# Performance work log

Measured on AMD Instinct MI355X. Metric: run time of the kernel, lower is better.

## Reference

```python
import jax, jax.numpy as jnp
import numpy as np

N_MELS = 80
FORMANT_START, FORMANT_END = 10, 50
W_L1, W_DELTA, W_DELTA2, W_SC, W_BAND, FORMANT_W = 1.0, 0.5, 0.25, 0.5, 1.0, 2.0
EPS = 1e-8


def _masked_mean(x, mask):
    # mask broadcasts to x's shape; count = sum of the broadcast mask
    n = jnp.maximum(jnp.sum(jnp.broadcast_to(mask, x.shape)), 1.0)
    return jnp.sum(x * mask) / n


def setup_inputs() -> dict:
    key = jax.random.key(0)
    k1, k2, k3 = jax.random.split(key, 3)
    B, T, D = 64, 4000, N_MELS
    pred_mel = jax.random.normal(k1, (B, T, D), dtype=jnp.float32)
    target_mel = jax.random.normal(k2, (B, T, D), dtype=jnp.float32)
    lengths = jax.random.randint(k3, (B,), T // 2, T + 1)
    mel_mask = (jnp.arange(T)[None, :] < lengths[:, None]).astype(jnp.float32)
    band_weights = jnp.ones((D,), dtype=jnp.float32).at[FORMANT_START:FORMANT_END].set(FORMANT_W)
    return {"pred_mel": pred_mel, "target_mel": target_mel, "mel_mask": mel_mask,
            "band_weights": band_weights}


def reference(pred_mel, target_mel, mel_mask, band_weights):
    mask3 = mel_mask[:, :, None]                      # (B,T,1)

    l1 = jnp.abs(pred_mel - target_mel)               # (B,T,D)
    l1_loss = _masked_mean(l1, mask3)

    # 1st-order deltas
    dp = pred_mel[:, 1:] - pred_mel[:, :-1]
    dt = target_mel[:, 1:] - target_mel[:, :-1]
    dmask = (mel_mask[:, 1:] * mel_mask[:, :-1])[:, :, None]
    delta_loss = _masked_mean(jnp.abs(dp - dt), dmask)

    # 2nd-order deltas
    d2p = dp[:, 1:] - dp[:, :-1]
    d2t = dt[:, 1:] - dt[:, :-1]
    d2mask = (mel_mask[:, 2:] * mel_mask[:, 1:-1] * mel_mask[:, :-2])[:, :, None]
    delta2_loss = _masked_mean(jnp.abs(d2p - d2t), d2mask)

    # spectral convergence
    diff = (pred_mel - target_mel) * mask3
    tgt_m = target_mel * mask3
    n = jnp.maximum(jnp.sum(jnp.broadcast_to(mask3, pred_mel.shape)), 1.0)
    sc_num = jnp.sqrt(jnp.sum(diff * diff) / n)
    sc_den = jnp.maximum(jnp.sqrt(jnp.sum(tgt_m * tgt_m) / n), EPS)
    sc_loss = sc_num / sc_den

    # band-weighted L1
    w = band_weights[None, None, :]
    band_loss = _masked_mean(l1 * w, mask3) / jnp.mean(band_weights)

    # energy (per-frame mean over mel bins)
    e_l1 = jnp.abs(pred_mel.mean(axis=-1) - target_mel.mean(axis=-1))  # (B,T)
    energy_loss = _masked_mean(e_l1, mel_mask)

    return (W_L1 * l1_loss + W_DELTA * delta_loss + W_DELTA2 * delta2_loss
            + W_SC * sc_loss + W_BAND * band_loss + 0.5 * energy_loss)
```

## Files before the change

kernel.cpp:

```cpp
#include <hip/hip_runtime.h>
#include <math.h>

#define D_MELS  80
#define T_DIM   4000
#define F4_ROW  20
#define NQ      10
#define NTHR    256
#define WPB     (NTHR / 64)
#define RPW     16
#define LDSROWS (RPW + 2)
#define MAXB    2048

#define WAVE_FENCE() do { __asm__ volatile("" ::: "memory"); \
                          __builtin_amdgcn_wave_barrier();    \
                          __asm__ volatile("" ::: "memory"); } while (0)


__global__ __launch_bounds__(NTHR) void mel_loss_main(
    const float* __restrict__ pred, const float* __restrict__ tgt,
    const float* __restrict__ mask, const float* __restrict__ w,
    float* __restrict__ partial, int BT, int total_waves)
{
    const int tid  = threadIdx.x;
    const int lane = tid & 63;
    const int qtr  = lane & 3;
    const int rw   = lane >> 2;
    const int wid  = tid >> 6;
    const int gwave = blockIdx.x * WPB + wid;

    const float4* p4 = (const float4*)pred;
    const float4* q4 = (const float4*)tgt;

    __shared__ float4 ebuf[WPB][LDSROWS * F4_ROW];
    __shared__ float  red[WPB][NQ];
    float4* my = ebuf[wid];

    float4 wv[5];
    #pragma unroll
    for (int k = 0; k < 5; ++k) wv[k] = ((const float4*)w)[qtr + 4 * k];

    float v_l1 = 0.f, v_band = 0.f, v_diff2 = 0.f, v_tgt2 = 0.f, v_energy = 0.f;
    float v_m = 0.f, v_d = 0.f, v_dm = 0.f, v_d2 = 0.f, v_d2m = 0.f;

    const int stride_rows = total_waves * RPW;

    for (int base = gwave * RPW; base < BT; base += stride_rows) {
        int r = base + rw;
        bool active = (r < BT);
        int rc = active ? r : (BT - 1);
        int t = rc % T_DIM;

        const float4* pr = p4 + (size_t)rc * F4_ROW + qtr;
        const float4* qr = q4 + (size_t)rc * F4_ROW + qtr;

        float4 ecur[5];
        float l1r = 0.f, bandr = 0.f, sqr = 0.f, t2r = 0.f, er = 0.f;
        #pragma unroll
        for (int k = 0; k < 5; ++k) {
            float4 e = make_float4(0.f, 0.f, 0.f, 0.f);
            if (active) {
                float4 p = pr[4 * k];
                float4 q = qr[4 * k];
                e.x = p.x - q.x; e.y = p.y - q.y;
                e.z = p.z - q.z; e.w = p.w - q.w;
                float a0 = fabsf(e.x), a1 = fabsf(e.y),
                      a2 = fabsf(e.z), a3 = fabsf(e.w);
                l1r   += a0 + a1 + a2 + a3;
                bandr += a0 * wv[k].x + a1 * wv[k].y + a2 * wv[k].z + a3 * wv[k].w;
                sqr   += e.x * e.x + e.y * e.y + e.z * e.z + e.w * e.w;
                t2r   += q.x * q.x + q.y * q.y + q.z * q.z + q.w * q.w;
                er    += e.x + e.y + e.z + e.w;
            }
            ecur[k] = e;
            my[(rw + 2) * F4_ROW + qtr + 4 * k] = e;
        }

        if (rw <= 1) {
            bool hvalid = active && (t >= 2);
            const float4* ph = pr - 2 * F4_ROW;
            const float4* qh = qr - 2 * F4_ROW;
            #pragma unroll
            for (int k = 0; k < 5; ++k) {
                float4 he = make_float4(0.f, 0.f, 0.f, 0.f);
                if (hvalid) {
                    float4 a = ph[4 * k];
                    float4 b = qh[4 * k];
                    he.x = a.x - b.x; he.y = a.y - b.y;
                    he.z = a.z - b.z; he.w = a.w - b.w;
                }
                my[rw * F4_ROW + qtr + 4 * k] = he;
            }
        }

        WAVE_FENCE();

        float mt = active ? mask[rc] : 0.f;
        float m1 = (active && t >= 1) ? mask[rc - 1] : 0.f;
        float m2 = (active && t >= 2) ? mask[rc - 2] : 0.f;
        float dmv  = mt * m1;
        float d2mv = dmv * m2;

        float dr = 0.f, d2r = 0.f;
        #pragma unroll
        for (int k = 0; k < 5; ++k) {
            float4 e = ecur[k];
            float4 f = my[(rw + 1) * F4_ROW + qtr + 4 * k];
            float4 g = my[rw * F4_ROW + qtr + 4 * k];
            dr  += fabsf(e.x - f.x) + fabsf(e.y - f.y)
                 + fabsf(e.z - f.z) + fabsf(e.w - f.w);
            d2r += fabsf(e.x - 2.f * f.x + g.x) + fabsf(e.y - 2.f * f.y + g.y)
                 + fabsf(e.z - 2.f * f.z + g.z) + fabsf(e.w - 2.f * f.w + g.w);
        }

        v_l1    += l1r * mt;
        v_band  += bandr * mt;
        v_diff2 += sqr * mt;
        v_tgt2  += t2r * mt;
        v_d     += dr * dmv;
        v_d2    += d2r * d2mv;

        er += __shfl_xor(er, 1, 64);
        er += __shfl_xor(er, 2, 64);
        if (qtr == 0) {
            v_energy += fabsf(er) * mt;
            v_m   += mt;
            v_dm  += dmv;
            v_d2m += d2mv;
        }

        WAVE_FENCE();
    }

    float vals[NQ] = {v_l1, v_band, v_diff2, v_tgt2, v_energy,
                      v_m, v_d, v_dm, v_d2, v_d2m};
    #pragma unroll
    for (int q = 0; q < NQ; ++q) {
        float v = vals[q];
        #pragma unroll
        for (int off = 32; off > 0; off >>= 1)
            v += __shfl_down(v, off, 64);
        vals[q] = v;
    }
    if (lane == 0) {
        #pragma unroll
        for (int q = 0; q < NQ; ++q) red[wid][q] = vals[q];
    }
    __syncthreads();
    if (tid < NQ) {
        float s = 0.f;
        #pragma unroll
        for (int wv2 = 0; wv2 < WPB; ++wv2) s += red[wv2][tid];
        partial[tid * MAXB + blockIdx.x] = s;
    }
}

__global__ __launch_bounds__(640) void mel_loss_finalize(
    const float* __restrict__ partial, const float* __restrict__ w,
    float* __restrict__ out, int nblk)
{
    const int tid = threadIdx.x;
    const int wv  = tid >> 6;
    const int lane = tid & 63;
    __shared__ float fin[NQ];

    float s = 0.f;
    for (int i = lane; i < nblk; i += 64) s += partial[wv * MAXB + i];
    #pragma unroll
    for (int off = 32; off > 0; off >>= 1) s += __shfl_down(s, off, 64);
    if (lane == 0) fin[wv] = s;
    __syncthreads();

    if (tid == 0) {
        float l1s = fin[0], bands = fin[1], diff2 = fin[2], tgt2 = fin[3];
        float energys = fin[4], ms = fin[5], ds = fin[6], dms = fin[7];
        float d2s = fin[8], d2ms = fin[9];

        float wsum = 0.f;
        for (int d = 0; d < D_MELS; ++d) wsum += w[d];
        float wmean = wsum / (float)D_MELS;

        float n1  = fmaxf(ms   * (float)D_MELS, 1.f);
        float nd  = fmaxf(dms  * (float)D_MELS, 1.f);
        float nd2 = fmaxf(d2ms * (float)D_MELS, 1.f);

        float l1_loss     = l1s / n1;
        float delta_loss  = ds / nd;
        float delta2_loss = d2s / nd2;
        float sc_num = sqrtf(diff2 / n1);
        float sc_den = fmaxf(sqrtf(tgt2 / n1), 1e-8f);
        float sc_loss = sc_num / sc_den;
        float band_loss = (bands / n1) / wmean;
        float energy_loss = (energys / (float)D_MELS) / fmaxf(ms, 1.f);

        out[0] = 1.0f * l1_loss + 0.5f * delta_loss + 0.25f * delta2_loss
               + 0.5f * sc_loss + 1.0f * band_loss + 0.5f * energy_loss;
    }
}

extern "C" void kernel_launch(void* const* d_in, const int* in_sizes, int n_in,
                              void* d_out, int out_size, void* d_ws, size_t ws_size,
                              hipStream_t stream) {
    const float* pred = (const float*)d_in[0];
    const float* tgt  = (const float*)d_in[1];
    const float* mask = (const float*)d_in[2];
    const float* w    = (const float*)d_in[3];
    int BT = in_sizes[2];
    float* partial = (float*)d_ws;

    int block_iters = (BT + WPB * RPW - 1) / (WPB * RPW);
    int grid = (block_iters + 1) / 2;
    if (grid > MAXB) grid = MAXB;
    if (grid < 1) grid = 1;
    int total_waves = grid * WPB;

    mel_loss_main<<<grid, NTHR, 0, stream>>>(pred, tgt, mask, w, partial, BT, total_waves);
    mel_loss_finalize<<<1, 640, 0, stream>>>(partial, w, (float*)d_out, grid);
}
```

Measured before the change: 204.1 us.

## Use nontemporal loads, batch row loads, move band weights to LDS, enlarge grid

Main row loads now use nontemporal loads, and all P and Q vectors are issued before any arithmetic, so more memory requests are in flight at once. Band weights move from per-thread registers into LDS, and the delta loop rereads the current row from LDS to reduce register pressure. A launch-bounds occupancy hint is added. The grid now launches one block per 64-row tile (capped at 4096) instead of two tiles per block. The aim is better latency hiding in this bandwidth-bound pass, at the cost of more blocks, more partials to reduce, and extra LDS reads.

```diff
diff --git a/kernel.cpp b/kernel.cpp
--- a/kernel.cpp
+++ b/kernel.cpp
@@ -9,14 +9,20 @@
 #define WPB     (NTHR / 64)
 #define RPW     16
 #define LDSROWS (RPW + 2)
-#define MAXB    2048
+#define MAXB    4096
+
+typedef float f4 __attribute__((ext_vector_type(4)));
+
+__device__ __forceinline__ f4 ntload(const f4* p) {
+    return __builtin_nontemporal_load(p);
+}
 
 #define WAVE_FENCE() do { __asm__ volatile("" ::: "memory"); \
                           __builtin_amdgcn_wave_barrier();    \
                           __asm__ volatile("" ::: "memory"); } while (0)
 
 
-__global__ __launch_bounds__(NTHR) void mel_loss_main(
+__global__ __launch_bounds__(NTHR, 5) void mel_loss_main(
     const float* __restrict__ pred, const float* __restrict__ tgt,
     const float* __restrict__ mask, const float* __restrict__ w,
     float* __restrict__ partial, int BT, int total_waves)
@@ -28,16 +34,16 @@
     const int wid  = tid >> 6;
     const int gwave = blockIdx.x * WPB + wid;
 
-    const float4* p4 = (const float4*)pred;
-    const float4* q4 = (const float4*)tgt;
-
-    __shared__ float4 ebuf[WPB][LDSROWS * F4_ROW];
-    __shared__ float  red[WPB][NQ];
-    float4* my = ebuf[wid];
-
-    float4 wv[5];
-    #pragma unroll
-    for (int k = 0; k < 5; ++k) wv[k] = ((const float4*)w)[qtr + 4 * k];
+    const f4* p4 = (const f4*)pred;
+    const f4* q4 = (const f4*)tgt;
+
+    __shared__ f4    wvb[F4_ROW];
+    __shared__ f4    ebuf[WPB][LDSROWS * F4_ROW];
+    __shared__ float red[WPB][NQ];
+    f4* my = ebuf[wid];
+
+    if (tid < F4_ROW) wvb[tid] = ((const f4*)w)[tid];
+    __syncthreads();
 
     float v_l1 = 0.f, v_band = 0.f, v_diff2 = 0.f, v_tgt2 = 0.f, v_energy = 0.f;
     float v_m = 0.f, v_d = 0.f, v_dm = 0.f, v_d2 = 0.f, v_d2m = 0.f;
@@ -50,62 +56,58 @@
         int rc = active ? r : (BT - 1);
         int t = rc % T_DIM;
 
-        const float4* pr = p4 + (size_t)rc * F4_ROW + qtr;
-        const float4* qr = q4 + (size_t)rc * F4_ROW + qtr;
-
-        float4 ecur[5];
-        float l1r = 0.f, bandr = 0.f, sqr = 0.f, t2r = 0.f, er = 0.f;
-        #pragma unroll
-        for (int k = 0; k < 5; ++k) {
-            float4 e = make_float4(0.f, 0.f, 0.f, 0.f);
-            if (active) {
-                float4 p = pr[4 * k];
-                float4 q = qr[4 * k];
-                e.x = p.x - q.x; e.y = p.y - q.y;
-                e.z = p.z - q.z; e.w = p.w - q.w;
-                float a0 = fabsf(e.x), a1 = fabsf(e.y),
-                      a2 = fabsf(e.z), a3 = fabsf(e.w);
-                l1r   += a0 + a1 + a2 + a3;
-                bandr += a0 * wv[k].x + a1 * wv[k].y + a2 * wv[k].z + a3 * wv[k].w;
-                sqr   += e.x * e.x + e.y * e.y + e.z * e.z + e.w * e.w;
-                t2r   += q.x * q.x + q.y * q.y + q.z * q.z + q.w * q.w;
-                er    += e.x + e.y + e.z + e.w;
-            }
-            ecur[k] = e;
-            my[(rw + 2) * F4_ROW + qtr + 4 * k] = e;
-        }
-
-        if (rw <= 1) {
-            bool hvalid = active && (t >= 2);
-            const float4* ph = pr - 2 * F4_ROW;
-            const float4* qh = qr - 2 * F4_ROW;
-            #pragma unroll
-            for (int k = 0; k < 5; ++k) {
-                float4 he = make_float4(0.f, 0.f, 0.f, 0.f);
-                if (hvalid) {
-                    float4 a = ph[4 * k];
-                    float4 b = qh[4 * k];
-                    he.x = a.x - b.x; he.y = a.y - b.y;
-                    he.z = a.z - b.z; he.w = a.w - b.w;
-                }
-                my[rw * F4_ROW + qtr + 4 * k] = he;
-            }
-        }
-
-        WAVE_FENCE();
+        const f4* pr = p4 + (size_t)rc * F4_ROW + qtr;
+        const f4* qr = q4 + (size_t)rc * F4_ROW + qtr;
 
         float mt = active ? mask[rc] : 0.f;
         float m1 = (active && t >= 1) ? mask[rc - 1] : 0.f;
         float m2 = (active && t >= 2) ? mask[rc - 2] : 0.f;
+
+        if (rw <= 1) {
+            bool hvalid = active && (t >= 2);
+            const f4* ph = pr - 2 * F4_ROW;
+            const f4* qh = qr - 2 * F4_ROW;
+            #pragma unroll
+            for (int k = 0; k < 5; ++k) {
+                f4 he = (f4)(0.f);
+                if (hvalid) he = ph[4 * k] - qh[4 * k];
+                my[rw * F4_ROW + qtr + 4 * k] = he;
+            }
+        }
+
+        f4 P[5], Q[5];
+        #pragma unroll
+        for (int k = 0; k < 5; ++k) P[k] = ntload(pr + 4 * k);
+        #pragma unroll
+        for (int k = 0; k < 5; ++k) Q[k] = ntload(qr + 4 * k);
+
+        float l1r = 0.f, bandr = 0.f, sqr = 0.f, t2r = 0.f, er = 0.f;
+        #pragma unroll
+        for (int k = 0; k < 5; ++k) {
+            f4 e = P[k] - Q[k];
+            f4 wv = wvb[qtr + 4 * k];
+            float a0 = fabsf(e.x), a1 = fabsf(e.y),
+                  a2 = fabsf(e.z), a3 = fabsf(e.w);
+            l1r   += a0 + a1 + a2 + a3;
+            bandr += a0 * wv.x + a1 * wv.y + a2 * wv.z + a3 * wv.w;
+            sqr   += e.x * e.x + e.y * e.y + e.z * e.z + e.w * e.w;
+            t2r   += Q[k].x * Q[k].x + Q[k].y * Q[k].y
+                   + Q[k].z * Q[k].z + Q[k].w * Q[k].w;
+            er    += e.x + e.y + e.z + e.w;
+            my[(rw + 2) * F4_ROW + qtr + 4 * k] = e;
+        }
+
+        WAVE_FENCE();
+
         float dmv  = mt * m1;
         float d2mv = dmv * m2;
 
         float dr = 0.f, d2r = 0.f;
         #pragma unroll
         for (int k = 0; k < 5; ++k) {
-            float4 e = ecur[k];
-            float4 f = my[(rw + 1) * F4_ROW + qtr + 4 * k];
-            float4 g = my[rw * F4_ROW + qtr + 4 * k];
+            f4 e = my[(rw + 2) * F4_ROW + qtr + 4 * k];
+            f4 f = my[(rw + 1) * F4_ROW + qtr + 4 * k];
+            f4 g = my[rw * F4_ROW + qtr + 4 * k];
             dr  += fabsf(e.x - f.x) + fabsf(e.y - f.y)
                  + fabsf(e.z - f.z) + fabsf(e.w - f.w);
             d2r += fabsf(e.x - 2.f * f.x + g.x) + fabsf(e.y - 2.f * f.y + g.y)
@@ -207,8 +209,8 @@
     int BT = in_sizes[2];
     float* partial = (float*)d_ws;
 
-    int block_iters = (BT + WPB * RPW - 1) / (WPB * RPW);
-    int grid = (block_iters + 1) / 2;
+    int rows_per_block = WPB * RPW;
+    int grid = (BT + rows_per_block - 1) / rows_per_block;
     if (grid > MAXB) grid = MAXB;
     if (grid < 1) grid = 1;
     int total_waves = grid * WPB;
```

Measured after the change: 298.5 us. +46.2%, slower.
